# Kernel tuning notes

Hardware: AMD Instinct MI355X
Metric: run time of the kernel (lower is better)

## Reference

```python
import jax, jax.numpy as jnp
import numpy as np

LOG_2PIE = float(np.log(2 * np.pi * np.e))


def _mu_logvar(inputs, targets, W_fe, b_fe, W_lv, b_lv):
    # inputs: [Nep, N, Din], targets: [Nep, N, 1]
    phis = jax.nn.relu(jnp.einsum('end,df->enf', inputs, W_fe) + b_fe)  # [Nep, N, D]
    x = jnp.concatenate([targets, phis], axis=-1)                        # [Nep, N, D+1]
    # z = cat(mean over shots, std over shots (unbiased, as torch.std))
    z = jnp.concatenate([jnp.mean(x, axis=1), jnp.std(x, axis=1, ddof=1)], axis=-1)  # [Nep, T]
    mu = z  # use_net_for_mu=False
    logvar = jnp.clip(z @ W_lv + b_lv, -9.0, -2.0)  # Linear + Hardtanh(-9,-2)
    return mu, logvar


def _pairwise_kl(mu1, lv1, mu2, lv2):
    # KL(N(mu1_i, lv1_i) || N(mu2_j, lv2_j)) for all (i, j): [Nep, Nep]
    m1, l1 = mu1[:, None, :], lv1[:, None, :]
    m2, l2 = mu2[None, :, :], lv2[None, :, :]
    t = l2 - l1 + (jnp.exp(l1) + (m1 - m2) ** 2) * jnp.exp(-l2) - 1.0
    return 0.5 * jnp.sum(t, axis=-1)


def reference(train_inputs, train_targets, test_inputs, test_targets, W_fe, b_fe, W_lv, b_lv):
    mu_tr, lv_tr = _mu_logvar(train_inputs, train_targets, W_fe, b_fe, W_lv, b_lv)
    mu_te, lv_te = _mu_logvar(test_inputs, test_targets, W_fe, b_fe, W_lv, b_lv)
    T = mu_tr.shape[-1]
    # normal_entropy as written in source: logvar.sum() + 0.5*d*log(2*pi*e)
    H_tr = jnp.sum(lv_tr, axis=-1) + 0.5 * T * LOG_2PIE  # [Nep]
    H_te = jnp.sum(lv_te, axis=-1) + 0.5 * T * LOG_2PIE  # [Nep]
    score = (_pairwise_kl(mu_tr, lv_tr, mu_te, lv_te)
             + _pairwise_kl(mu_te, lv_te, mu_tr, lv_tr).T
             + H_tr[:, None] + H_te[None, :])
    probs = jax.nn.log_softmax(-score, axis=1)
    classes = jnp.arange(score.shape[0], dtype=jnp.int64 if jax.config.jax_enable_x64 else jnp.int32)
    return probs, classes


def setup_inputs() -> dict:
    key = jax.random.key(0)
    ks = jax.random.split(key, 6)
    Nep, N, Din, D = 256, 32, 512, 512
    T = 2 * (D + 1)
    return {
        'train_inputs': jax.random.normal(ks[0], (Nep, N, Din), jnp.float32),
        'train_targets': jax.random.normal(ks[1], (Nep, N, 1), jnp.float32),
        'test_inputs': jax.random.normal(ks[2], (Nep, N, Din), jnp.float32),
        'test_targets': jax.random.normal(ks[3], (Nep, N, 1), jnp.float32),
        'W_fe': jax.random.normal(ks[4], (Din, D), jnp.float32) / np.sqrt(Din),
        'b_fe': jnp.zeros((D,), jnp.float32),
        'W_lv': jax.random.normal(ks[5], (T, T), jnp.float32) / np.sqrt(T),
        'b_lv': jnp.zeros((T,), jnp.float32),
    }
```

## Files before the change

### kernel.cpp

```cpp
#include <hip/hip_runtime.h>
#include <math.h>

#define TDIM 1026
#define KP 1056
#define NP 1152
#define KSPLIT 7
#define KK 4224

typedef __attribute__((ext_vector_type(8))) short bf16x8;
typedef __attribute__((ext_vector_type(4))) float f32x4;

__device__ inline unsigned int pk_bf16(float a, float b) {
    unsigned int ua = __float_as_uint(a), ub = __float_as_uint(b);
    ua = (ua + 0x7FFFu + ((ua >> 16) & 1u)) >> 16;
    ub = (ub + 0x7FFFu + ((ub >> 16) & 1u)) & 0xFFFF0000u;
    return ua | ub;
}
__device__ inline unsigned short f2bf(float a) {
    unsigned int ua = __float_as_uint(a);
    return (unsigned short)((ua + 0x7FFFu + ((ua >> 16) & 1u)) >> 16);
}

__global__ __launch_bounds__(256)
void k_cvtboth(const float* __restrict__ Wfe, const float* __restrict__ Wlv,
               unsigned short* __restrict__ Wt, unsigned short* __restrict__ Wlt,
               const float* __restrict__ Ttr, const float* __restrict__ Tte,
               float* __restrict__ Z, unsigned short* __restrict__ Zb,
               float* __restrict__ Hs_te, float* __restrict__ cterm)
{
    __shared__ float T[32][33];
    const int z = blockIdx.z;
    const int t = threadIdx.x;
    if (z == 2) {
        if (blockIdx.y != 0 || blockIdx.x >= 2) return;
        if (blockIdx.x == 0) { Hs_te[t] = 0.f; cterm[t] = 0.f; }
        int e = blockIdx.x * 256 + t;
        const float* p = (e < 256) ? (Ttr + (size_t)e * 32) : (Tte + (size_t)(e - 256) * 32);
        float S1 = 0.f, S2 = 0.f;
#pragma unroll
        for (int n = 0; n < 32; ++n) { float v = p[n]; S1 += v; S2 += v * v; }
        float mean = S1 * (1.f / 32.f);
        float var  = (S2 - 32.f * mean * mean) * (1.f / 31.f);
        float sd   = sqrtf(fmaxf(var, 0.f));
        Z[(size_t)e * TDIM + 0]   = mean;
        Z[(size_t)e * TDIM + 513] = sd;
        Zb[(size_t)e * KP + 0]    = f2bf(mean);
        Zb[(size_t)e * KP + 513]  = f2bf(sd);
#pragma unroll
        for (int c = TDIM; c < KP; ++c) Zb[(size_t)e * KP + c] = 0;
        return;
    }
    if (z && (blockIdx.x >= 16 || blockIdx.y >= 16)) return;
    const float* W = z ? Wfe : Wlv;
    unsigned short* D = z ? Wt : Wlt;
    const int S  = z ? 512 : TDIM;
    const int DS = z ? 512 : KP;
    const int n0 = blockIdx.x * 32, k0 = blockIdx.y * 32;
    {
        int ky = t >> 3, nx = (t & 7) * 4;
#pragma unroll
        for (int i = 0; i < 4; ++i) {
            float v = 0.f;
            if (k0 + ky < S && n0 + nx + i < S)
                v = W[(size_t)(k0 + ky) * S + n0 + nx + i];
            T[nx + i][ky] = v;
        }
    }
    __syncthreads();
    {
        int ny = t >> 3, kx = (t & 7) * 4;
        ushort4 o;
        o.x = f2bf(T[ny][kx + 0]); o.y = f2bf(T[ny][kx + 1]);
        o.z = f2bf(T[ny][kx + 2]); o.w = f2bf(T[ny][kx + 3]);
        *(ushort4*)(D + (size_t)(n0 + ny) * DS + k0 + kx) = o;
    }
}

__global__ __launch_bounds__(256)
void k_fe_mfma(const float* __restrict__ Atr, const float* __restrict__ Ate,
               const unsigned short* __restrict__ Wt,
               const float* __restrict__ bfe, float* __restrict__ Z,
               unsigned short* __restrict__ Zb)
{
    __shared__ unsigned short As[2][64 * 40];
    __shared__ unsigned short Bs[2][128 * 40];
    __shared__ float2 sbuf[2 * 128];

    const int tid  = threadIdx.x;
    const int lane = tid & 63;
    const int wave = tid >> 6;
    const int m = lane & 15, quad = lane >> 4;
    const int row0 = blockIdx.x * 64;
    const int col0 = blockIdx.y * 128;
    const float* A = (row0 < 8192) ? Atr : Ate;
    const int ar0 = row0 & 8191;

    f32x4 acc[4][2];
#pragma unroll
    for (int i = 0; i < 4; ++i)
#pragma unroll
        for (int j = 0; j < 2; ++j) acc[i][j] = (f32x4){0.f, 0.f, 0.f, 0.f};

    const int srA = tid >> 2, skA = tid & 3;
    const int srB = tid >> 1, skB = tid & 1;

    float4 pa0, pa1;
    uint4  pb0, pb1;

#define FE_PRELOAD(K0)                                                          \
    {                                                                           \
        const float* ap = A + (size_t)(ar0 + srA) * 512 + (K0) + skA * 8;       \
        pa0 = *(const float4*)(ap);                                             \
        pa1 = *(const float4*)(ap + 4);                                         \
        const unsigned short* bp = Wt + (size_t)(col0 + srB) * 512 + (K0) + skB * 16; \
        pb0 = *(const uint4*)(bp);                                              \
        pb1 = *(const uint4*)(bp + 8);                                          \
    }
#define FE_WRITE(BUF)                                                           \
    {                                                                           \
        uint4 va;                                                               \
        va.x = pk_bf16(pa0.x, pa0.y); va.y = pk_bf16(pa0.z, pa0.w);             \
        va.z = pk_bf16(pa1.x, pa1.y); va.w = pk_bf16(pa1.z, pa1.w);             \
        *(uint4*)(As[BUF] + srA * 40 + skA * 8) = va;                           \
        *(uint4*)(Bs[BUF] + srB * 40 + skB * 16)     = pb0;                     \
        *(uint4*)(Bs[BUF] + srB * 40 + skB * 16 + 8) = pb1;                     \
    }

    FE_PRELOAD(0)
    FE_WRITE(0)
    FE_PRELOAD(32)
    __syncthreads();

    int cur = 0;
    for (int k0 = 0; k0 < 512; k0 += 32) {
        if (k0 + 32 < 512) {
            FE_WRITE(cur ^ 1)
            if (k0 + 64 < 512) FE_PRELOAD(k0 + 64)
        }
        bf16x8 af[4], bfr[2];
#pragma unroll
        for (int ti = 0; ti < 4; ++ti)
            af[ti] = *(const bf16x8*)(As[cur] + (ti * 16 + m) * 40 + quad * 8);
#pragma unroll
        for (int tj = 0; tj < 2; ++tj)
            bfr[tj] = *(const bf16x8*)(Bs[cur] + (wave * 32 + tj * 16 + m) * 40 + quad * 8);
#pragma unroll
        for (int ti = 0; ti < 4; ++ti)
#pragma unroll
            for (int tj = 0; tj < 2; ++tj)
                acc[ti][tj] = __builtin_amdgcn_mfma_f32_16x16x32_bf16(
                    af[ti], bfr[tj], acc[ti][tj], 0, 0, 0);
        __syncthreads();
        cur ^= 1;
    }

#pragma unroll
    for (int ep = 0; ep < 2; ++ep) {
#pragma unroll
        for (int tj = 0; tj < 2; ++tj) {
            int colL = wave * 32 + tj * 16 + m;
            float b = bfe[col0 + colL];
            float s1 = 0.f, s2 = 0.f;
#pragma unroll
            for (int p = 0; p < 2; ++p) {
                int ti = ep * 2 + p;
#pragma unroll
                for (int r = 0; r < 4; ++r) {
                    float v = fmaxf(acc[ti][tj][r] + b, 0.f);
                    s1 += v; s2 += v * v;
                }
            }
            s1 += __shfl_xor(s1, 16); s1 += __shfl_xor(s1, 32);
            s2 += __shfl_xor(s2, 16); s2 += __shfl_xor(s2, 32);
            if (lane < 16) sbuf[ep * 128 + colL] = make_float2(s1, s2);
        }
    }
    __syncthreads();
    {
        int ep = tid >> 7, cl = tid & 127;
        float2 pr = sbuf[ep * 128 + cl];
        float mean = pr.x * (1.f / 32.f);
        float var  = (pr.y - 32.f * mean * mean) * (1.f / 31.f);
        float sd   = sqrtf(fmaxf(var, 0.f));
        int e = blockIdx.x * 2 + ep;
        int f = col0 + cl;
        Z[(size_t)e * TDIM + 1 + f]   = mean;
        Z[(size_t)e * TDIM + 514 + f] = sd;
        Zb[(size_t)e * KP + 1 + f]    = f2bf(mean);
        Zb[(size_t)e * KP + 514 + f]  = f2bf(sd);
    }
}

__global__ __launch_bounds__(256)
void k_lv_mfma(const unsigned short* __restrict__ Zb,
               const unsigned short* __restrict__ Wlt,
               float* __restrict__ Cacc)
{
    __shared__ unsigned short As[128 * 40];
    __shared__ unsigned short Bs[128 * 40];

    const int tid  = threadIdx.x;
    const int lane = tid & 63;
    const int wave = tid >> 6;
    const int wr = wave >> 1, wc = wave & 1;
    const int m = lane & 15, quad = lane >> 4;
    const int col0 = blockIdx.x * 128;
    const int row0 = blockIdx.y * 128;
    const int p    = blockIdx.z;
    const int it0  = (p < 5) ? p * 5 : 25 + (p - 5) * 4;
    const int itn  = (p < 5) ? 5 : 4;

    f32x4 acc[4][4];
#pragma unroll
    for (int i = 0; i < 4; ++i)
#pragma unroll
        for (int j = 0; j < 4; ++j) acc[i][j] = (f32x4){0.f, 0.f, 0.f, 0.f};

    const int srow = tid >> 2;
    const int skc  = tid & 3;

    for (int it = it0; it < it0 + itn; ++it) {
        int k0 = it * 32;
#pragma unroll
        for (int s = 0; s < 2; ++s) {
            int row = srow + s * 64;
            uint4 va = *(const uint4*)(Zb  + (size_t)(row0 + row) * KP + k0 + skc * 8);
            uint4 vb = *(const uint4*)(Wlt + (size_t)(col0 + row) * KP + k0 + skc * 8);
            *(uint4*)(As + row * 40 + skc * 8) = va;
            *(uint4*)(Bs + row * 40 + skc * 8) = vb;
        }
        __syncthreads();
        bf16x8 af[4], bfr[4];
#pragma unroll
        for (int t2 = 0; t2 < 4; ++t2) {
            af[t2]  = *(const bf16x8*)(As + (wr * 64 + t2 * 16 + m) * 40 + quad * 8);
            bfr[t2] = *(const bf16x8*)(Bs + (wc * 64 + t2 * 16 + m) * 40 + quad * 8);
        }
#pragma unroll
        for (int ti = 0; ti < 4; ++ti)
#pragma unroll
            for (int tj = 0; tj < 4; ++tj)
                acc[ti][tj] = __builtin_amdgcn_mfma_f32_16x16x32_bf16(
                    af[ti], bfr[tj], acc[ti][tj], 0, 0, 0);
        __syncthreads();
    }

    float* C = Cacc + (size_t)p * 512 * NP;
#pragma unroll
    for (int ti = 0; ti < 4; ++ti)
#pragma unroll
        for (int tj = 0; tj < 4; ++tj) {
            int c = col0 + wc * 64 + tj * 16 + m;
#pragma unroll
            for (int r = 0; r < 4; ++r) {
                int rg = row0 + wr * 64 + ti * 16 + quad * 4 + r;
                C[(size_t)rg * NP + c] = acc[ti][tj][r];
            }
        }
}

__global__ __launch_bounds__(256)
void k_lv_ep(const float* __restrict__ Cacc, const float* __restrict__ Zf,
             const float* __restrict__ blv,
             unsigned short* __restrict__ Xb, unsigned short* __restrict__ Yb,
             float* __restrict__ Hs_te, float* __restrict__ cterm)
{
    const int t = threadIdx.x;
    const int rl = t >> 3;
    const int ci = t & 7;
    const int r  = blockIdx.y * 32 + rl;
    const int c0 = blockIdx.x * 32 + ci * 4;
    const bool is_te = (r >= 256);

    float4 s = make_float4(0.f, 0.f, 0.f, 0.f);
#pragma unroll
    for (int p = 0; p < KSPLIT; ++p) {
        float4 v = *(const float4*)(Cacc + (size_t)p * 512 * NP + (size_t)r * NP + c0);
        s.x += v.x; s.y += v.y; s.z += v.z; s.w += v.w;
    }
    float sv[4] = {s.x, s.y, s.z, s.w};

    unsigned short* O = is_te ? (Yb + (size_t)(r - 256) * KK) : (Xb + (size_t)r * KK);
    float h = 0.f, ct = 0.f;
#pragma unroll
    for (int q = 0; q < 4; ++q) {
        int c = c0 + q;
        bool cok = (c < TDIM);
        ushort4 o = make_ushort4(0, 0, 0, 0);
        if (cok) {
            float x = fminf(fmaxf(sv[q] + blv[c], -9.f), -2.f);
            float E = expf(x);
            float R = expf(-x);
            float mm = Zf[(size_t)r * TDIM + c];
            if (!is_te) {
                o.x = f2bf(E + mm * mm);
                o.y = f2bf(R);
                o.z = f2bf(-2.f * mm * R);
                o.w = f2bf(-2.f * mm);
            } else {
                o.x = f2bf(R);
                o.y = f2bf(E + mm * mm);
                o.z = f2bf(mm);
                o.w = f2bf(mm * R);
                h  += x;
                ct += mm * mm * R;
            }
        }
        *(ushort4*)(O + 4 * c) = o;
    }
    if (is_te) {
        h  += __shfl_xor(h, 1);  h  += __shfl_xor(h, 2);  h  += __shfl_xor(h, 4);
        ct += __shfl_xor(ct, 1); ct += __shfl_xor(ct, 2); ct += __shfl_xor(ct, 4);
        if (ci == 0) {
            atomicAdd(Hs_te + (r - 256), h);
            atomicAdd(cterm + (r - 256), ct);
        }
    }
}

__global__ __launch_bounds__(256)
void k_pgemm(const unsigned short* __restrict__ Xb,
             const unsigned short* __restrict__ Yb,
             float* __restrict__ Sp)
{
    __shared__ unsigned short As[128 * 40];
    __shared__ unsigned short Bs[128 * 40];

    const int tid  = threadIdx.x;
    const int lane = tid & 63;
    const int wave = tid >> 6;
    const int wr = wave >> 1, wc = wave & 1;
    const int m = lane & 15, quad = lane >> 4;
    const int col0 = blockIdx.x * 128;
    const int row0 = blockIdx.y * 128;
    const int p    = blockIdx.z;
    const int it0  = (p < 4) ? p * 9 : 36 + (p - 4) * 8;
    const int itn  = (p < 4) ? 9 : 8;

    f32x4 acc[4][4];
#pragma unroll
    for (int i = 0; i < 4; ++i)
#pragma unroll
        for (int j = 0; j < 4; ++j) acc[i][j] = (f32x4){0.f, 0.f, 0.f, 0.f};

    const int srow = tid >> 2;
    const int skc  = tid & 3;

    for (int it = it0; it < it0 + itn; ++it) {
        int k0 = it * 32;
#pragma unroll
        for (int s = 0; s < 2; ++s) {
            int row = srow + s * 64;
            uint4 va = *(const uint4*)(Xb + (size_t)(row0 + row) * KK + k0 + skc * 8);
            uint4 vb = *(const uint4*)(Yb + (size_t)(col0 + row) * KK + k0 + skc * 8);
            *(uint4*)(As + row * 40 + skc * 8) = va;
            *(uint4*)(Bs + row * 40 + skc * 8) = vb;
        }
        __syncthreads();
        bf16x8 af[4], bfr[4];
#pragma unroll
        for (int t2 = 0; t2 < 4; ++t2) {
            af[t2]  = *(const bf16x8*)(As + (wr * 64 + t2 * 16 + m) * 40 + quad * 8);
            bfr[t2] = *(const bf16x8*)(Bs + (wc * 64 + t2 * 16 + m) * 40 + quad * 8);
        }
#pragma unroll
        for (int ti = 0; ti < 4; ++ti)
#pragma unroll
            for (int tj = 0; tj < 4; ++tj)
                acc[ti][tj] = __builtin_amdgcn_mfma_f32_16x16x32_bf16(
                    af[ti], bfr[tj], acc[ti][tj], 0, 0, 0);
        __syncthreads();
    }

    float* C = Sp + (size_t)p * 65536;
#pragma unroll
    for (int ti = 0; ti < 4; ++ti)
#pragma unroll
        for (int tj = 0; tj < 4; ++tj) {
            int c = col0 + wc * 64 + tj * 16 + m;
#pragma unroll
            for (int r = 0; r < 4; ++r) {
                int rg = row0 + wr * 64 + ti * 16 + quad * 4 + r;
                C[(size_t)rg * 256 + c] = acc[ti][tj][r];
            }
        }
}

__global__ __launch_bounds__(256)
void k_soft(const float* __restrict__ Sp, const float* __restrict__ Hs_te,
            const float* __restrict__ cterm, float* __restrict__ outp)
{
    __shared__ float red[4], red2[4];
    const int i = blockIdx.x, j = threadIdx.x;
    float s = 0.f;
#pragma unroll
    for (int tc = 0; tc < 16; ++tc)
        s += Sp[((size_t)tc * 256 + i) * 256 + j];
    float v = -(0.5f * (s + cterm[j]) + Hs_te[j]);

    float m = v;
#pragma unroll
    for (int o = 32; o > 0; o >>= 1) m = fmaxf(m, __shfl_xor(m, o));
    if ((j & 63) == 0) red[j >> 6] = m;
    __syncthreads();
    m = fmaxf(fmaxf(red[0], red[1]), fmaxf(red[2], red[3]));

    float p = v - m;
    float t = expf(p);
#pragma unroll
    for (int o = 32; o > 0; o >>= 1) t += __shfl_xor(t, o);
    if ((j & 63) == 0) red2[j >> 6] = t;
    __syncthreads();
    t = red2[0] + red2[1] + red2[2] + red2[3];

    outp[(size_t)i * 256 + j] = p - logf(t);
    if (i == 0) outp[65536 + j] = (float)j;
}

__global__ __launch_bounds__(256)
void k_fe_f32(const float* __restrict__ Atr, const float* __restrict__ Ate,
              const float* __restrict__ Wfe, const float* __restrict__ bfe,
              float* __restrict__ Z, float* __restrict__ muT_te)
{
    __shared__ float lds[4224];
    float* Ast = lds;
    float* Bs  = lds + 2112;
    const int tid = threadIdx.x;
    const int tx = tid & 15;
    const int ty = tid >> 4;
    const int col0 = blockIdx.x * 128;
    const int row0 = blockIdx.y * 128;
    const float* A = (row0 < 8192) ? Atr : Ate;
    const int ar0 = (row0 < 8192) ? row0 : (row0 - 8192);

    float acc[8][8];
#pragma unroll
    for (int i = 0; i < 8; ++i)
#pragma unroll
        for (int j = 0; j < 8; ++j) acc[i][j] = 0.f;

    for (int k0 = 0; k0 < 512; k0 += 16) {
#pragma unroll
        for (int s = 0; s < 2; ++s) {
            int u = tid + s * 256;
            int row = u >> 2, q = u & 3;
            float4 v = *(const float4*)(A + (size_t)(ar0 + row) * 512 + k0 + q * 4);
            Ast[(q * 4 + 0) * 132 + row] = v.x;
            Ast[(q * 4 + 1) * 132 + row] = v.y;
            Ast[(q * 4 + 2) * 132 + row] = v.z;
            Ast[(q * 4 + 3) * 132 + row] = v.w;
        }
#pragma unroll
        for (int s = 0; s < 2; ++s) {
            int u = tid + s * 256;
            int kk = u >> 5, c8 = u & 31;
            float4 v = *(const float4*)(Wfe + (size_t)(k0 + kk) * 512 + col0 + c8 * 4);
            *(float4*)(Bs + kk * 132 + c8 * 4) = v;
        }
        __syncthreads();
#pragma unroll
        for (int kk = 0; kk < 16; ++kk) {
            float4 a0 = *(const float4*)(Ast + kk * 132 + ty * 8);
            float4 a1 = *(const float4*)(Ast + kk * 132 + ty * 8 + 4);
            float4 b0 = *(const float4*)(Bs + kk * 132 + tx * 4);
            float4 b1 = *(const float4*)(Bs + kk * 132 + 64 + tx * 4);
            float av[8] = {a0.x, a0.y, a0.z, a0.w, a1.x, a1.y, a1.z, a1.w};
            float bv[8] = {b0.x, b0.y, b0.z, b0.w, b1.x, b1.y, b1.z, b1.w};
#pragma unroll
            for (int i = 0; i < 8; ++i)
#pragma unroll
                for (int j = 0; j < 8; ++j)
                    acc[i][j] = fmaf(av[i], bv[j], acc[i][j]);
        }
        __syncthreads();
    }

    float2* sbuf = (float2*)lds;
#pragma unroll
    for (int j = 0; j < 8; ++j) {
        int cl = (j < 4) ? (tx * 4 + j) : (64 + tx * 4 + (j - 4));
        float b = bfe[col0 + cl];
        float s1 = 0.f, s2 = 0.f;
#pragma unroll
        for (int i = 0; i < 8; ++i) {
            float v = acc[i][j] + b;
            v = fmaxf(v, 0.f);
            s1 += v; s2 += v * v;
        }
        sbuf[ty * 128 + cl] = make_float2(s1, s2);
    }
    __syncthreads();
    for (int idx = tid; idx < 512; idx += 256) {
        int ep = idx >> 7, cl = idx & 127;
        float S1 = 0.f, S2 = 0.f;
#pragma unroll
        for (int q = 0; q < 4; ++q) {
            float2 p = sbuf[(ep * 4 + q) * 128 + cl];
            S1 += p.x; S2 += p.y;
        }
        float mean = S1 * (1.f / 32.f);
        float var  = (S2 - 32.f * mean * mean) * (1.f / 31.f);
        float sd   = sqrtf(fmaxf(var, 0.f));
        int e = (row0 >> 5) + ep;
        int f = col0 + cl;
        Z[(size_t)e * TDIM + 1 + f]   = mean;
        Z[(size_t)e * TDIM + 514 + f] = sd;
        if (e >= 256) {
            int j2 = e - 256;
            muT_te[(size_t)(1 + f) * 256 + j2]   = mean;
            muT_te[(size_t)(514 + f) * 256 + j2] = sd;
        }
    }
}

__global__ __launch_bounds__(256)
void k_tgt_f32(const float* __restrict__ Ttr, const float* __restrict__ Tte,
               float* __restrict__ Z, float* __restrict__ muT_te,
               float* __restrict__ Hs_te)
{
    if (blockIdx.x == 0) Hs_te[threadIdx.x] = 0.f;
    int e = blockIdx.x * 256 + threadIdx.x;
    if (e >= 512) return;
    const float* p = (e < 256) ? (Ttr + (size_t)e * 32) : (Tte + (size_t)(e - 256) * 32);
    float S1 = 0.f, S2 = 0.f;
#pragma unroll
    for (int n = 0; n < 32; ++n) { float v = p[n]; S1 += v; S2 += v * v; }
    float mean = S1 * (1.f / 32.f);
    float var  = (S2 - 32.f * mean * mean) * (1.f / 31.f);
    float sd   = sqrtf(fmaxf(var, 0.f));
    Z[(size_t)e * TDIM + 0]   = mean;
    Z[(size_t)e * TDIM + 513] = sd;
    if (e >= 256) {
        muT_te[(size_t)0 * 256 + (e - 256)]   = mean;
        muT_te[(size_t)513 * 256 + (e - 256)] = sd;
    }
}

__global__ __launch_bounds__(256)
void k_lv(const float* __restrict__ Z, const float* __restrict__ Wlv,
          const float* __restrict__ blv,
          float* __restrict__ E_tr, float* __restrict__ R_tr,
          float* __restrict__ E_teT, float* __restrict__ R_teT,
          float* __restrict__ Hs_te)
{
    __shared__ float Ast[16 * 68];
    __shared__ float Bs[16 * 68];
    const int tid = threadIdx.x;
    const int tx = tid & 15;
    const int ty = tid >> 4;
    const int col0 = blockIdx.x * 64;
    const int row0 = blockIdx.y * 64;

    float acc[4][4];
#pragma unroll
    for (int i = 0; i < 4; ++i)
#pragma unroll
        for (int j = 0; j < 4; ++j) acc[i][j] = 0.f;

    for (int k0 = 0; k0 < TDIM; k0 += 16) {
        {
            int row = tid >> 2, kp = tid & 3;
            const float* src = Z + (size_t)(row0 + row) * TDIM + k0 + kp * 4;
            float x0 = 0.f, x1 = 0.f, x2 = 0.f, x3 = 0.f;
            if (k0 + kp * 4 + 1 < TDIM) { float2 v = *(const float2*)(src);     x0 = v.x; x1 = v.y; }
            if (k0 + kp * 4 + 3 < TDIM) { float2 v = *(const float2*)(src + 2); x2 = v.x; x3 = v.y; }
            Ast[(kp * 4 + 0) * 68 + row] = x0;
            Ast[(kp * 4 + 1) * 68 + row] = x1;
            Ast[(kp * 4 + 2) * 68 + row] = x2;
            Ast[(kp * 4 + 3) * 68 + row] = x3;
        }
        {
            int kk = tid >> 4, cg = tid & 15;
#pragma unroll
            for (int c = 0; c < 4; ++c) {
                int col = col0 + cg * 4 + c;
                float v = 0.f;
                if (k0 + kk < TDIM && col < TDIM)
                    v = Wlv[(size_t)(k0 + kk) * TDIM + col];
                Bs[kk * 68 + cg * 4 + c] = v;
            }
        }
        __syncthreads();
#pragma unroll
        for (int kk = 0; kk < 16; ++kk) {
            float4 a = *(const float4*)(Ast + kk * 68 + ty * 4);
            float4 b = *(const float4*)(Bs + kk * 68 + tx * 4);
            float av[4] = {a.x, a.y, a.z, a.w};
            float bv[4] = {b.x, b.y, b.z, b.w};
#pragma unroll
            for (int i = 0; i < 4; ++i)
#pragma unroll
                for (int j = 0; j < 4; ++j)
                    acc[i][j] = fmaf(av[i], bv[j], acc[i][j]);
        }
        __syncthreads();
    }

    float hpart[4] = {0.f, 0.f, 0.f, 0.f};
#pragma unroll
    for (int i = 0; i < 4; ++i) {
        int r = row0 + ty * 4 + i;
#pragma unroll
        for (int j = 0; j < 4; ++j) {
            int c = col0 + tx * 4 + j;
            if (c < TDIM) {
                float lv = acc[i][j] + blv[c];
                lv = fminf(fmaxf(lv, -9.f), -2.f);
                float E = expf(lv);
                float R = expf(-lv);
                if (r < 256) {
                    E_tr[(size_t)r * TDIM + c] = E;
                    R_tr[(size_t)r * TDIM + c] = R;
                } else {
                    E_teT[(size_t)c * 256 + (r - 256)] = E;
                    R_teT[(size_t)c * 256 + (r - 256)] = R;
                    hpart[i] += lv;
                }
            }
        }
    }
    if (row0 >= 256) {
        __syncthreads();
        float* hbuf = Ast;
#pragma unroll
        for (int i = 0; i < 4; ++i) hbuf[(ty * 4 + i) * 16 + tx] = hpart[i];
        __syncthreads();
        if (tid < 64) {
            float s = 0.f;
#pragma unroll
            for (int x = 0; x < 16; ++x) s += hbuf[tid * 16 + x];
            atomicAdd(Hs_te + (row0 - 256 + tid), s);
        }
    }
}

#define TCH 65
__global__ __launch_bounds__(256)
void k_pair(const float* __restrict__ Z, const float* __restrict__ E_tr,
            const float* __restrict__ R_tr, const float* __restrict__ muT_te,
            const float* __restrict__ E_teT, const float* __restrict__ R_teT,
            float* __restrict__ Sp)
{
    __shared__ float Lm[8 * 68], Le[8 * 68], Lr[8 * 68];
    const int tid = threadIdx.x;
    const int i0 = blockIdx.x * 8;
    const int t0 = blockIdx.y * TCH;
    const int tlen = min(TCH, TDIM - t0);

    if (tid < tlen) {
#pragma unroll
        for (int r = 0; r < 8; ++r) {
            size_t off = (size_t)(i0 + r) * TDIM + t0 + tid;
            Lm[r * 68 + tid] = Z[off];
            Le[r * 68 + tid] = E_tr[off];
            Lr[r * 68 + tid] = R_tr[off];
        }
    }
    __syncthreads();

    float S[8];
#pragma unroll
    for (int r = 0; r < 8; ++r) S[r] = 0.f;
    const int j = tid;
    for (int tt = 0; tt < tlen; ++tt) {
        size_t o = (size_t)(t0 + tt) * 256 + j;
        float m2 = muT_te[o], e2 = E_teT[o], r2 = R_teT[o];
#pragma unroll
        for (int r = 0; r < 8; ++r) {
            float m1 = Lm[r * 68 + tt];
            float e1 = Le[r * 68 + tt];
            float r1 = Lr[r * 68 + tt];
            float d = m1 - m2;
            S[r] += e1 * r2 + e2 * r1 + d * d * (r1 + r2);
        }
    }
#pragma unroll
    for (int r = 0; r < 8; ++r)
        Sp[((size_t)blockIdx.y * 256 + i0 + r) * 256 + j] = S[r];
}

__global__ __launch_bounds__(256)
void k_soft_fb(const float* __restrict__ Sp, const float* __restrict__ Hs_te,
               float* __restrict__ outp)
{
    __shared__ float red[4], red2[4];
    const int i = blockIdx.x, j = threadIdx.x;
    float s = 0.f;
#pragma unroll
    for (int tc = 0; tc < 16; ++tc)
        s += Sp[((size_t)tc * 256 + i) * 256 + j];
    float v = -(0.5f * s + Hs_te[j]);

    float m = v;
#pragma unroll
    for (int o = 32; o > 0; o >>= 1) m = fmaxf(m, __shfl_xor(m, o));
    if ((j & 63) == 0) red[j >> 6] = m;
    __syncthreads();
    m = fmaxf(fmaxf(red[0], red[1]), fmaxf(red[2], red[3]));

    float p = v - m;
    float t = expf(p);
#pragma unroll
    for (int o = 32; o > 0; o >>= 1) t += __shfl_xor(t, o);
    if ((j & 63) == 0) red2[j >> 6] = t;
    __syncthreads();
    t = red2[0] + red2[1] + red2[2] + red2[3];

    outp[(size_t)i * 256 + j] = p - logf(t);
    if (i == 0) outp[65536 + j] = (float)j;
}

extern "C" void kernel_launch(void* const* d_in, const int* in_sizes, int n_in,
                              void* d_out, int out_size, void* d_ws, size_t ws_size,
                              hipStream_t stream)
{
    const float* tri = (const float*)d_in[0];
    const float* trt = (const float*)d_in[1];
    const float* tei = (const float*)d_in[2];
    const float* tet = (const float*)d_in[3];
    const float* Wfe = (const float*)d_in[4];
    const float* bfe = (const float*)d_in[5];
    const float* Wlv = (const float*)d_in[6];
    const float* blv = (const float*)d_in[7];
    float* outp = (float*)d_out;

    char* base = (char*)d_ws;
    float* Z     = (float*)base;
    float* Sp    = (float*)(base + 2101248);
    float* Hs_te = (float*)(base + 2101248 + 4194304);
    float* cterm = (float*)(base + 2101248 + 4194304 + 1024);
    float* Cacc  = (float*)(base + 6296576 + 1024);
    unsigned short* Wt = (unsigned short*)(base + 6297600 + 16515072);
    unsigned short* Xb = (unsigned short*)(base + 22812672 + 524288);
    unsigned short* Yb = (unsigned short*)(base + 23336960 + 2162688);
    unsigned short* Wlt = (unsigned short*)Sp;
    unsigned short* Zb  = (unsigned short*)((char*)Sp + 2433024);

    const size_t need = 23336960ull + 2162688ull + 2162688ull;
    const bool fast = (ws_size >= need);

    if (fast) {
        k_cvtboth<<<dim3(36, 33, 3), 256, 0, stream>>>(Wfe, Wlv, Wt, Wlt,
                                                       trt, tet, Z, Zb, Hs_te, cterm);
        k_fe_mfma<<<dim3(256, 4), 256, 0, stream>>>(tri, tei, Wt, bfe, Z, Zb);
        k_lv_mfma<<<dim3(9, 4, KSPLIT), 256, 0, stream>>>(Zb, Wlt, Cacc);
        k_lv_ep  <<<dim3(33, 16), 256, 0, stream>>>(Cacc, Z, blv, Xb, Yb, Hs_te, cterm);
        k_pgemm  <<<dim3(2, 2, 16), 256, 0, stream>>>(Xb, Yb, Sp);
        k_soft   <<<256, 256, 0, stream>>>(Sp, Hs_te, cterm, outp);
    } else {
        float* Zf    = (float*)d_ws;
        float* E_tr  = Zf + (size_t)512 * TDIM;
        float* R_tr  = E_tr + (size_t)256 * TDIM;
        float* muT   = R_tr + (size_t)256 * TDIM;
        float* E_teT = muT + (size_t)TDIM * 256;
        float* R_teT = E_teT + (size_t)TDIM * 256;
        float* Hs    = R_teT + (size_t)TDIM * 256;
        float* Spf   = Hs + 256;
        k_fe_f32 <<<dim3(4, 128), 256, 0, stream>>>(tri, tei, Wfe, bfe, Zf, muT);
        k_tgt_f32<<<2, 256, 0, stream>>>(trt, tet, Zf, muT, Hs);
        k_lv     <<<dim3(17, 8), 256, 0, stream>>>(Zf, Wlv, blv, E_tr, R_tr, E_teT, R_teT, Hs);
        k_pair   <<<dim3(32, 16), 256, 0, stream>>>(Zf, E_tr, R_tr, muT, E_teT, R_teT, Spf);
        k_soft_fb<<<256, 256, 0, stream>>>(Spf, Hs, outp);
    }
}
```

Before: 139.4 us.

## Load MFMA fragments directly from global memory, dropping LDS staging in three GEMMs

In the feature-extraction, logvar and pairwise GEMM kernels, each wave now loads its MFMA operand fragments straight from global memory into registers. Shared-memory staging and the __syncthreads barriers are gone, replaced by a register-level software prefetch of the next K-slice. This removes LDS write/read traffic and block-wide synchronisation. The cost is that operands shared between waves are fetched redundantly from global/L2 memory, and access is less coalesced (16-byte strided rows per lane) with higher register pressure.

```diff
diff --git a/kernel.cpp b/kernel.cpp
--- a/kernel.cpp
+++ b/kernel.cpp
@@ -19,6 +19,15 @@
 __device__ inline unsigned short f2bf(float a) {
     unsigned int ua = __float_as_uint(a);
     return (unsigned short)((ua + 0x7FFFu + ((ua >> 16) & 1u)) >> 16);
+}
+__device__ inline bf16x8 cvt8(const float4& a, const float4& b) {
+    union { uint4 u; bf16x8 h; } cv;
+    cv.u.x = pk_bf16(a.x, a.y); cv.u.y = pk_bf16(a.z, a.w);
+    cv.u.z = pk_bf16(b.x, b.y); cv.u.w = pk_bf16(b.z, b.w);
+    return cv.h;
+}
+__device__ inline bf16x8 asbf8(const uint4& v) {
+    union { uint4 u; bf16x8 h; } cv; cv.u = v; return cv.h;
 }
 
 __global__ __launch_bounds__(256)
@@ -82,8 +91,6 @@
                const float* __restrict__ bfe, float* __restrict__ Z,
                unsigned short* __restrict__ Zb)
 {
-    __shared__ unsigned short As[2][64 * 40];
-    __shared__ unsigned short Bs[2][128 * 40];
     __shared__ float2 sbuf[2 * 128];
 
     const int tid  = threadIdx.x;
@@ -95,63 +102,46 @@
     const float* A = (row0 < 8192) ? Atr : Ate;
     const int ar0 = row0 & 8191;
 
+    const float* ap0 = A + (size_t)(ar0 + m) * 512 + quad * 8;
+    const unsigned short* bp0 = Wt + (size_t)(col0 + wave * 32 + m) * 512 + quad * 8;
+
     f32x4 acc[4][2];
 #pragma unroll
     for (int i = 0; i < 4; ++i)
 #pragma unroll
         for (int j = 0; j < 2; ++j) acc[i][j] = (f32x4){0.f, 0.f, 0.f, 0.f};
 
-    const int srA = tid >> 2, skA = tid & 3;
-    const int srB = tid >> 1, skB = tid & 1;
-
-    float4 pa0, pa1;
-    uint4  pb0, pb1;
-
-#define FE_PRELOAD(K0)                                                          \
-    {                                                                           \
-        const float* ap = A + (size_t)(ar0 + srA) * 512 + (K0) + skA * 8;       \
-        pa0 = *(const float4*)(ap);                                             \
-        pa1 = *(const float4*)(ap + 4);                                         \
-        const unsigned short* bp = Wt + (size_t)(col0 + srB) * 512 + (K0) + skB * 16; \
-        pb0 = *(const uint4*)(bp);                                              \
-        pb1 = *(const uint4*)(bp + 8);                                          \
-    }
-#define FE_WRITE(BUF)                                                           \
-    {                                                                           \
-        uint4 va;                                                               \
-        va.x = pk_bf16(pa0.x, pa0.y); va.y = pk_bf16(pa0.z, pa0.w);             \
-        va.z = pk_bf16(pa1.x, pa1.y); va.w = pk_bf16(pa1.z, pa1.w);             \
-        *(uint4*)(As[BUF] + srA * 40 + skA * 8) = va;                           \
-        *(uint4*)(Bs[BUF] + srB * 40 + skB * 16)     = pb0;                     \
-        *(uint4*)(Bs[BUF] + srB * 40 + skB * 16 + 8) = pb1;                     \
-    }
-
-    FE_PRELOAD(0)
-    FE_WRITE(0)
-    FE_PRELOAD(32)
-    __syncthreads();
-
-    int cur = 0;
+    float4 pa[4][2];
+    uint4  pb[2];
+
+#define FE_LOAD(K0)                                                     \
+    {                                                                   \
+        _Pragma("unroll")                                               \
+        for (int ti = 0; ti < 4; ++ti) {                                \
+            const float* p = ap0 + ti * 16 * 512 + (K0);                \
+            pa[ti][0] = *(const float4*)(p);                            \
+            pa[ti][1] = *(const float4*)(p + 4);                        \
+        }                                                               \
+        _Pragma("unroll")                                               \
+        for (int tj = 0; tj < 2; ++tj)                                  \
+            pb[tj] = *(const uint4*)(bp0 + tj * 16 * 512 + (K0));       \
+    }
+
+    FE_LOAD(0)
+#pragma unroll
     for (int k0 = 0; k0 < 512; k0 += 32) {
-        if (k0 + 32 < 512) {
-            FE_WRITE(cur ^ 1)
-            if (k0 + 64 < 512) FE_PRELOAD(k0 + 64)
-        }
         bf16x8 af[4], bfr[2];
 #pragma unroll
-        for (int ti = 0; ti < 4; ++ti)
-            af[ti] = *(const bf16x8*)(As[cur] + (ti * 16 + m) * 40 + quad * 8);
-#pragma unroll
-        for (int tj = 0; tj < 2; ++tj)
-            bfr[tj] = *(const bf16x8*)(Bs[cur] + (wave * 32 + tj * 16 + m) * 40 + quad * 8);
+        for (int ti = 0; ti < 4; ++ti) af[ti] = cvt8(pa[ti][0], pa[ti][1]);
+#pragma unroll
+        for (int tj = 0; tj < 2; ++tj) bfr[tj] = asbf8(pb[tj]);
+        if (k0 + 32 < 512) FE_LOAD(k0 + 32)
 #pragma unroll
         for (int ti = 0; ti < 4; ++ti)
 #pragma unroll
             for (int tj = 0; tj < 2; ++tj)
                 acc[ti][tj] = __builtin_amdgcn_mfma_f32_16x16x32_bf16(
                     af[ti], bfr[tj], acc[ti][tj], 0, 0, 0);
-        __syncthreads();
-        cur ^= 1;
     }
 
 #pragma unroll
@@ -196,9 +186,6 @@
                const unsigned short* __restrict__ Wlt,
                float* __restrict__ Cacc)
 {
-    __shared__ unsigned short As[128 * 40];
-    __shared__ unsigned short Bs[128 * 40];
-
     const int tid  = threadIdx.x;
     const int lane = tid & 63;
     const int wave = tid >> 6;
@@ -210,39 +197,39 @@
     const int it0  = (p < 5) ? p * 5 : 25 + (p - 5) * 4;
     const int itn  = (p < 5) ? 5 : 4;
 
+    const unsigned short* ap0 = Zb  + (size_t)(row0 + wr * 64 + m) * KP + quad * 8;
+    const unsigned short* bp0 = Wlt + (size_t)(col0 + wc * 64 + m) * KP + quad * 8;
+
     f32x4 acc[4][4];
 #pragma unroll
     for (int i = 0; i < 4; ++i)
 #pragma unroll
         for (int j = 0; j < 4; ++j) acc[i][j] = (f32x4){0.f, 0.f, 0.f, 0.f};
 
-    const int srow = tid >> 2;
-    const int skc  = tid & 3;
-
-    for (int it = it0; it < it0 + itn; ++it) {
-        int k0 = it * 32;
-#pragma unroll
-        for (int s = 0; s < 2; ++s) {
-            int row = srow + s * 64;
-            uint4 va = *(const uint4*)(Zb  + (size_t)(row0 + row) * KP + k0 + skc * 8);
-            uint4 vb = *(const uint4*)(Wlt + (size_t)(col0 + row) * KP + k0 + skc * 8);
-            *(uint4*)(As + row * 40 + skc * 8) = va;
-            *(uint4*)(Bs + row * 40 + skc * 8) = vb;
-        }
-        __syncthreads();
+    uint4 pa[4], pb[4];
+#define LV_LOAD(K0)                                                     \
+    {                                                                   \
+        _Pragma("unroll")                                               \
+        for (int t2 = 0; t2 < 4; ++t2) {                                \
+            pa[t2] = *(const uint4*)(ap0 + t2 * 16 * KP + (K0));        \
+            pb[t2] = *(const uint4*)(bp0 + t2 * 16 * KP + (K0));        \
+        }                                                               \
+    }
+
+    int k0 = it0 * 32;
+    const int kend = (it0 + itn) * 32;
+    LV_LOAD(k0)
+    for (; k0 < kend; k0 += 32) {
         bf16x8 af[4], bfr[4];
 #pragma unroll
-        for (int t2 = 0; t2 < 4; ++t2) {
-            af[t2]  = *(const bf16x8*)(As + (wr * 64 + t2 * 16 + m) * 40 + quad * 8);
-            bfr[t2] = *(const bf16x8*)(Bs + (wc * 64 + t2 * 16 + m) * 40 + quad * 8);
-        }
+        for (int t2 = 0; t2 < 4; ++t2) { af[t2] = asbf8(pa[t2]); bfr[t2] = asbf8(pb[t2]); }
+        if (k0 + 32 < kend) LV_LOAD(k0 + 32)
 #pragma unroll
         for (int ti = 0; ti < 4; ++ti)
 #pragma unroll
             for (int tj = 0; tj < 4; ++tj)
                 acc[ti][tj] = __builtin_amdgcn_mfma_f32_16x16x32_bf16(
                     af[ti], bfr[tj], acc[ti][tj], 0, 0, 0);
-        __syncthreads();
     }
 
     float* C = Cacc + (size_t)p * 512 * NP;
@@ -323,9 +310,6 @@
              const unsigned short* __restrict__ Yb,
              float* __restrict__ Sp)
 {
-    __shared__ unsigned short As[128 * 40];
-    __shared__ unsigned short Bs[128 * 40];
-
     const int tid  = threadIdx.x;
     const int lane = tid & 63;
     const int wave = tid >> 6;
@@ -337,39 +321,39 @@
     const int it0  = (p < 4) ? p * 9 : 36 + (p - 4) * 8;
     const int itn  = (p < 4) ? 9 : 8;
 
+    const unsigned short* ap0 = Xb + (size_t)(row0 + wr * 64 + m) * KK + quad * 8;
+    const unsigned short* bp0 = Yb + (size_t)(col0 + wc * 64 + m) * KK + quad * 8;
+
     f32x4 acc[4][4];
 #pragma unroll
     for (int i = 0; i < 4; ++i)
 #pragma unroll
         for (int j = 0; j < 4; ++j) acc[i][j] = (f32x4){0.f, 0.f, 0.f, 0.f};
 
-    const int srow = tid >> 2;
-    const int skc  = tid & 3;
-
-    for (int it = it0; it < it0 + itn; ++it) {
-        int k0 = it * 32;
-#pragma unroll
-        for (int s = 0; s < 2; ++s) {
-            int row = srow + s * 64;
-            uint4 va = *(const uint4*)(Xb + (size_t)(row0 + row) * KK + k0 + skc * 8);
-            uint4 vb = *(const uint4*)(Yb + (size_t)(col0 + row) * KK + k0 + skc * 8);
-            *(uint4*)(As + row * 40 + skc * 8) = va;
-            *(uint4*)(Bs + row * 40 + skc * 8) = vb;
-        }
-        __syncthreads();
+    uint4 pa[4], pb[4];
+#define PG_LOAD(K0)                                                     \
+    {                                                                   \
+        _Pragma("unroll")                                               \
+        for (int t2 = 0; t2 < 4; ++t2) {                                \
+            pa[t2] = *(const uint4*)(ap0 + t2 * 16 * KK + (K0));        \
+            pb[t2] = *(const uint4*)(bp0 + t2 * 16 * KK + (K0));        \
+        }                                                               \
+    }
+
+    int k0 = it0 * 32;
+    const int kend = (it0 + itn) * 32;
+    PG_LOAD(k0)
+    for (; k0 < kend; k0 += 32) {
         bf16x8 af[4], bfr[4];
 #pragma unroll
-        for (int t2 = 0; t2 < 4; ++t2) {
-            af[t2]  = *(const bf16x8*)(As + (wr * 64 + t2 * 16 + m) * 40 + quad * 8);
-            bfr[t2] = *(const bf16x8*)(Bs + (wc * 64 + t2 * 16 + m) * 40 + quad * 8);
-        }
+        for (int t2 = 0; t2 < 4; ++t2) { af[t2] = asbf8(pa[t2]); bfr[t2] = asbf8(pb[t2]); }
+        if (k0 + 32 < kend) PG_LOAD(k0 + 32)
 #pragma unroll
         for (int ti = 0; ti < 4; ++ti)
 #pragma unroll
             for (int tj = 0; tj < 4; ++tj)
                 acc[ti][tj] = __builtin_amdgcn_mfma_f32_16x16x32_bf16(
                     af[ti], bfr[tj], acc[ti][tj], 0, 0, 0);
-        __syncthreads();
     }
 
     float* C = Sp + (size_t)p * 65536;
```

Result: slower. 190.0 us (+36.3%).
